# Kernel tuning notes

Hardware: AMD Instinct MI355X
Metric: run time of the kernel (lower is better)

## Reference

```python
import jax, jax.numpy as jnp
import numpy as np

B, NQ, NK, C = 16, 8, 4096, 256
H = W = 64
HEADS = 8
CI = 128          # embedding_dim // attention_downsample_rate
HD = CI // HEADS  # per-head dim
EPS = float(np.finfo(np.float32).tiny)


def _gumbel_topk(scores, noise, n):
    # iterative gumbel-softmax top-k relaxation with straight-through hard k-hot
    g = scores + noise
    khot = jnp.zeros_like(g)
    onehot = jnp.zeros_like(g)
    for _ in range(n):
        g = g + jnp.log(jnp.maximum(1.0 - onehot, EPS))
        onehot = jax.nn.softmax(g, axis=-1)
        khot = khot + onehot
    _, ind = jax.lax.top_k(khot, n)
    rows = jnp.arange(khot.shape[0])[:, None]
    hard = jnp.zeros_like(khot).at[rows, ind].set(1.0)
    ret = hard - jax.lax.stop_gradient(khot) + khot  # == hard numerically
    return ret, jnp.sort(ind, axis=1)  # sorted idx = row-major order of boolean-mask select


def _sample_points(pe, content, ret, idx):
    # pe [H,W,C], content [b,H,W,C], ret [b,HW] k-hot, idx [b,k] sorted
    b = ret.shape[0]
    m = ret.reshape(b, H, W, 1)
    pe_m = (pe[None] * m).reshape(b, H * W, -1)
    c_m = (content * m).reshape(b, H * W, -1)
    take = lambda a: jnp.take_along_axis(a, idx[:, :, None], axis=1)
    return take(pe_m), take(c_m)


def _mlp(x, W1, b1, W2, b2, W3, b3):
    x = jax.nn.relu(x @ W1 + b1)
    x = jax.nn.relu(x @ W2 + b2)
    return x @ W3 + b3


def _forward(queries, keys, query_pe, key_pe, guiding_embedding, gumbel_p, gumbel_n,
             static_uncertain, static_refined, Wq, bq, Wk, bk, Wv, bv, Wo, bo,
             uW1, ub1, uW2, ub2, uW3, ub3, rW1, rb1, rW2, rb2, rW3, rb3,
             pe_gauss, point_pos, point_neg, n_sample_points):
    b = queries.shape[0]
    g = guiding_embedding.reshape(b, C, H * W).transpose(0, 2, 1)  # [b, HW, C]
    g = g * keys  # elementwise gating -> new guiding embedding

    # cross attention token -> image (internal dim CI, HEADS heads)
    def split_heads(x, Wx, bx):
        return (x @ Wx + bx).reshape(b, -1, HEADS, HD).transpose(0, 2, 1, 3)
    qh = split_heads(queries + query_pe, Wq, bq)
    kh = split_heads(g + key_pe, Wk, bk)
    vh = split_heads(g, Wv, bv)
    attn = jax.nn.softmax(jnp.einsum('bhqd,bhkd->bhqk', qh, kh) / np.float32(np.sqrt(HD)), axis=-1)
    out = jnp.einsum('bhqk,bhkd->bhqd', attn, vh).transpose(0, 2, 1, 3).reshape(b, -1, CI)
    queries = out @ Wo + bo  # [b, NQ, C]

    q1 = queries[:, 1, :]
    unc_tok = _mlp(jnp.concatenate([jnp.broadcast_to(static_uncertain, (b, C)), q1], -1),
                   uW1, ub1, uW2, ub2, uW3, ub3)
    ref_tok = _mlp(jnp.concatenate([jnp.broadcast_to(static_refined, (b, C)), q1], -1),
                   rW1, rb1, rW2, rb2, rW3, rb3)

    img = g.transpose(0, 2, 1)  # [b, C, HW]
    unc_norm = jax.nn.sigmoid(jnp.einsum('bc,bcn->bn', unc_tok, img))
    ref_mask = jnp.einsum('bc,bcn->bn', ref_tok, img)
    coarse_mask = jnp.einsum('bc,bcn->bn', q1, img)

    queries = jnp.concatenate([queries[:, 0:1], ref_tok[:, None, :], queries[:, 2:]], axis=1)

    # point-sampling reference map + gumbel-softmax top-k (training-path math)
    ref_map = unc_norm * (jax.nn.sigmoid(ref_mask) - jax.nn.sigmoid(coarse_mask))  # [b, HW]
    ret_p, idx_p = _gumbel_topk(ref_map, gumbel_p, n_sample_points)
    ret_n, idx_n = _gumbel_topk(-ref_map, gumbel_n, n_sample_points)

    # random fourier positional encoding of the 64x64 grid (SAM PositionEmbeddingRandom)
    xs = (jnp.arange(W, dtype=jnp.float32) + 0.5) / W
    ys = (jnp.arange(H, dtype=jnp.float32) + 0.5) / H
    coords = jnp.stack([jnp.tile(xs[None, :], (H, 1)), jnp.tile(ys[:, None], (1, W))], axis=-1)
    proj = ((2.0 * coords - 1.0) @ pe_gauss) * np.float32(2.0 * np.pi)  # [H, W, C//2]
    pe = jnp.concatenate([jnp.sin(proj), jnp.cos(proj)], axis=-1)       # [H, W, C]

    # F.interpolate of a 64x64 map to (64,64) is the identity here
    content = (keys + g).reshape(b, H, W, C)

    sp_pe, sp_c = _sample_points(pe, content, ret_p, idx_p)
    sn_pe, sn_c = _sample_points(pe, content, ret_n, idx_n)
    sp_pe = sp_pe + point_pos  # prompt_encoder.point_embeddings[1]
    sn_pe = sn_pe + point_neg  # prompt_encoder.point_embeddings[0]

    query_pe = jnp.concatenate([query_pe, sp_pe, sn_pe], axis=1)
    queries = jnp.concatenate([queries, sp_c, sn_c], axis=1)
    # pack (queries, query_pe) into one array for a single-output reference
    return jnp.concatenate([queries, query_pe], axis=1)  # [b, 2*(NQ+2k), C]


def setup_inputs():
    key = jax.random.key(0)
    ks = iter(jax.random.split(key, 48))
    n = lambda shape, s=1.0: jax.random.normal(next(ks), shape, jnp.float32) * s
    z = lambda shape: jnp.zeros(shape, jnp.float32)
    return {
        'queries': n((B, NQ, C)),
        'keys': n((B, NK, C)),
        'query_pe': n((B, NQ, C)),
        'key_pe': n((B, NK, C)),
        'guiding_embedding': n((B, C, H, W)),
        'gumbel_p': jax.random.gumbel(next(ks), (B, NK), jnp.float32),
        'gumbel_n': jax.random.gumbel(next(ks), (B, NK), jnp.float32),
        'static_uncertain': n((C,), 0.02),
        'static_refined': n((C,), 0.02),
        'Wq': n((C, CI), 0.02), 'bq': z((CI,)),
        'Wk': n((C, CI), 0.02), 'bk': z((CI,)),
        'Wv': n((C, CI), 0.02), 'bv': z((CI,)),
        'Wo': n((CI, C), 0.02), 'bo': z((C,)),
        'uW1': n((2 * C, C // 4), 0.05), 'ub1': z((C // 4,)),
        'uW2': n((C // 4, C // 4), 0.05), 'ub2': z((C // 4,)),
        'uW3': n((C // 4, C), 0.05), 'ub3': z((C,)),
        'rW1': n((2 * C, C // 4), 0.05), 'rb1': z((C // 4,)),
        'rW2': n((C // 4, C // 4), 0.05), 'rb2': z((C // 4,)),
        'rW3': n((C // 4, C), 0.05), 'rb3': z((C,)),
        'pe_gauss': n((2, C // 2)),
        'point_pos': n((C,), 0.02),
        'point_neg': n((C,), 0.02),
        'n_sample_points': 4,
    }


def reference(queries, keys, query_pe, key_pe, guiding_embedding, gumbel_p, gumbel_n,
              static_uncertain, static_refined, Wq, bq, Wk, bk, Wv, bv, Wo, bo,
              uW1, ub1, uW2, ub2, uW3, ub3, rW1, rb1, rW2, rb2, rW3, rb3,
              pe_gauss, point_pos, point_neg, n_sample_points):
    return _forward(queries, keys, query_pe, key_pe, guiding_embedding, gumbel_p, gumbel_n,
                    static_uncertain, static_refined, Wq, bq, Wk, bk, Wv, bv, Wo, bo,
                    uW1, ub1, uW2, ub2, uW3, ub3, rW1, rb1, rW2, rb2, rW3, rb3,
                    pe_gauss, point_pos, point_neg, n_sample_points)
```

## Files before the change

### kernel.cpp

```cpp
#include <hip/hip_runtime.h>

#define BB 16
#define NQn 8
#define NK 4096
#define CC 256
#define NHEADS 8
#define CIn 128
#define HDn 16
#define NHQ 64
#define EPS_TINY 1.17549435e-38f

constexpr size_t OFF_QK   = 0;
constexpr size_t OFF_QBK  = OFF_QK  + (size_t)BB*CC*NHQ;
constexpr size_t OFF_SC   = OFF_QBK + (size_t)BB*NHQ;
constexpr size_t OFF_MP   = OFF_SC  + (size_t)BB*NK*NHQ;
constexpr size_t OFF_SP   = OFF_MP  + (size_t)BB*16*NHQ;
constexpr size_t OFF_M    = OFF_SP  + (size_t)BB*16*NHQ;
constexpr size_t OFF_RS   = OFF_M   + (size_t)BB*NHQ;
constexpr size_t OFF_AVP  = OFF_RS  + (size_t)BB*NHQ;
constexpr size_t OFF_QATT = OFF_AVP + (size_t)BB*16*NHQ*CC;
constexpr size_t OFF_UNC  = OFF_QATT+ (size_t)BB*NQn*CC;
constexpr size_t OFF_REFT = OFF_UNC + (size_t)BB*CC;
constexpr size_t OFF_RMAP = OFF_REFT+ (size_t)BB*CC;
constexpr size_t OFF_IDX  = OFF_RMAP+ (size_t)BB*NK;
constexpr size_t OFF_RV   = OFF_IDX + 128;
constexpr size_t OFF_G    = OFF_RV  + 128;

__global__ __launch_bounds__(256) void t0_g(
    const float* __restrict__ keys, const float* __restrict__ guiding,
    float* __restrict__ ws)
{
  int bc = blockIdx.y; int b = bc >> 2; int c0 = (bc & 3) * 64;
  int n0 = blockIdx.x * 64; int t = threadIdx.x;
  __shared__ float Gt[64][65];
  int lane = t & 63, grp = t >> 6;
  #pragma unroll
  for (int cc = 0; cc < 16; ++cc) {
    int c = grp*16 + cc;
    Gt[c][lane] = guiding[((size_t)b*CC + c0 + c)*NK + n0 + lane];
  }
  __syncthreads();
  float* G = ws + OFF_G;
  int c4 = (t & 15) * 4, rowg = t >> 4;
  #pragma unroll
  for (int p = 0; p < 4; ++p) {
    int row = p*16 + rowg;
    size_t base = ((size_t)b*NK + n0 + row)*CC + c0 + c4;
    float4 kv = *(const float4*)&keys[base];
    float4 o;
    o.x = kv.x * Gt[c4+0][row];
    o.y = kv.y * Gt[c4+1][row];
    o.z = kv.z * Gt[c4+2][row];
    o.w = kv.w * Gt[c4+3][row];
    *(float4*)&G[base] = o;
  }
}

__global__ __launch_bounds__(256) void k1_qside(
    const float* __restrict__ queries, const float* __restrict__ query_pe,
    const float* __restrict__ Wq, const float* __restrict__ bq,
    const float* __restrict__ Wk, const float* __restrict__ bk,
    float* __restrict__ ws)
{
  int b = blockIdx.x >> 3, q = blockIdx.x & 7, t = threadIdx.x;
  __shared__ float x[CC];
  __shared__ float qh[CIn];
  x[t] = queries[(b*NQn+q)*CC + t] + query_pe[(b*NQn+q)*CC + t];
  __syncthreads();
  if (t < CIn) {
    float a = bq[t];
    for (int c = 0; c < CC; ++c) a += x[c]*Wq[c*CIn + t];
    qh[t] = a * 0.25f;
  }
  __syncthreads();
  float* Qk = ws + OFF_QK;
  #pragma unroll
  for (int h = 0; h < NHEADS; ++h) {
    float a = 0.f;
    #pragma unroll
    for (int d = 0; d < HDn; ++d) a += qh[h*HDn+d] * Wk[t*CIn + h*HDn + d];
    Qk[((size_t)b*CC + t)*NHQ + h*NQn + q] = a;
  }
  if (t < NHEADS) {
    float a = 0.f;
    #pragma unroll
    for (int d = 0; d < HDn; ++d) a += qh[t*HDn+d] * bk[t*HDn+d];
    (ws + OFF_QBK)[b*NHQ + t*NQn + q] = a;
  }
}

__global__ __launch_bounds__(256) void k2_scores(
    const float* __restrict__ key_pe, float* __restrict__ ws)
{
  int b = blockIdx.y, n0 = blockIdx.x * 64, t = threadIdx.x;
  __shared__ __align__(16) float Xs[64][68];
  __shared__ __align__(16) float Qs[64][64];
  const float* Qk = ws + OFF_QK;
  const float* G  = ws + OFF_G;
  int tx = t & 15, ty = t >> 4;
  int c4 = (t & 15)*4, rowg = t >> 4;
  float acc[4][4] = {};
  for (int c0 = 0; c0 < CC; c0 += 64) {
    __syncthreads();
    #pragma unroll
    for (int p = 0; p < 4; ++p) {
      int row = p*16 + rowg;
      size_t base = ((size_t)b*NK + n0 + row)*CC + c0 + c4;
      float4 gv = *(const float4*)&G[base];
      float4 pv = *(const float4*)&key_pe[base];
      float4 o; o.x = gv.x+pv.x; o.y = gv.y+pv.y; o.z = gv.z+pv.z; o.w = gv.w+pv.w;
      *(float4*)&Xs[row][c4] = o;
    }
    #pragma unroll
    for (int i = 0; i < 16; ++i) {
      int l = i*256 + t;
      Qs[l >> 6][l & 63] = Qk[((size_t)b*CC + c0 + (l>>6))*NHQ + (l & 63)];
    }
    __syncthreads();
    #pragma unroll 4
    for (int cb = 0; cb < 16; ++cb) {
      float4 xf[4], qf[4];
      #pragma unroll
      for (int i = 0; i < 4; ++i) xf[i] = *(const float4*)&Xs[4*ty+i][4*cb];
      #pragma unroll
      for (int u = 0; u < 4; ++u) qf[u] = *(const float4*)&Qs[4*cb+u][4*tx];
      #pragma unroll
      for (int u = 0; u < 4; ++u) {
        float xu[4] = { ((const float*)&xf[0])[u], ((const float*)&xf[1])[u],
                        ((const float*)&xf[2])[u], ((const float*)&xf[3])[u] };
        float qu[4] = { qf[u].x, qf[u].y, qf[u].z, qf[u].w };
        #pragma unroll
        for (int i = 0; i < 4; ++i)
          #pragma unroll
          for (int j = 0; j < 4; ++j) acc[i][j] += xu[i]*qu[j];
      }
    }
  }
  const float* qbk = ws + OFF_QBK + (size_t)b*NHQ;
  float qb[4] = {qbk[4*tx], qbk[4*tx+1], qbk[4*tx+2], qbk[4*tx+3]};
  float* sc = ws + OFF_SC + ((size_t)b*NK + n0)*NHQ;
  #pragma unroll
  for (int i = 0; i < 4; ++i) {
    float4 o;
    o.x = acc[i][0]+qb[0]; o.y = acc[i][1]+qb[1]; o.z = acc[i][2]+qb[2]; o.w = acc[i][3]+qb[3];
    *(float4*)&sc[(4*ty + i)*NHQ + 4*tx] = o;
  }
}

__global__ __launch_bounds__(256) void k3a_stats(float* __restrict__ ws)
{
  int b = blockIdx.y, sb = blockIdx.x, t = threadIdx.x;
  int hq = t & 63, r = t >> 6;
  const float* sc = ws + OFF_SC + ((size_t)b*NK + sb*256)*NHQ;
  float m = -INFINITY, s = 0.f;
  for (int i = 0; i < 64; ++i) {
    float v = sc[(r + 4*i)*NHQ + hq];
    if (v > m) { s = s*expf(m - v) + 1.f; m = v; } else { s += expf(v - m); }
  }
  __shared__ float rm[256], rs[256];
  rm[t] = m; rs[t] = s;
  __syncthreads();
  if (t < 64) {
    float m0=rm[t], m1=rm[t+64], m2=rm[t+128], m3=rm[t+192];
    float mm = fmaxf(fmaxf(m0,m1), fmaxf(m2,m3));
    float ss = rs[t]*expf(m0-mm) + rs[t+64]*expf(m1-mm) + rs[t+128]*expf(m2-mm) + rs[t+192]*expf(m3-mm);
    (ws + OFF_MP)[(b*16 + sb)*NHQ + t] = mm;
    (ws + OFF_SP)[(b*16 + sb)*NHQ + t] = ss;
  }
}

__global__ __launch_bounds__(64) void k3b_combine(float* __restrict__ ws)
{
  int b = blockIdx.x, hq = threadIdx.x;
  const float* mp = ws + OFF_MP + (size_t)b*16*NHQ;
  const float* sp = ws + OFF_SP + (size_t)b*16*NHQ;
  float m = -INFINITY;
  #pragma unroll
  for (int i = 0; i < 16; ++i) m = fmaxf(m, mp[i*NHQ+hq]);
  float s = 0.f;
  #pragma unroll
  for (int i = 0; i < 16; ++i) s += sp[i*NHQ+hq]*expf(mp[i*NHQ+hq]-m);
  (ws+OFF_M)[b*NHQ+hq] = m;
  (ws+OFF_RS)[b*NHQ+hq] = 1.0f/s;
}

__global__ __launch_bounds__(256) void k4_av(float* __restrict__ ws)
{
  int b = blockIdx.y, kb = blockIdx.x, t = threadIdx.x;
  int k0 = kb * 256;
  __shared__ __align__(16) float gld[32][260];
  __shared__ __align__(16) float wld[32][64];
  __shared__ float mv[64], rv[64];
  if (t < 64) { mv[t] = (ws+OFF_M)[b*NHQ+t]; rv[t] = (ws+OFF_RS)[b*NHQ+t]; }
  int th = t & 15, tc = t >> 4;
  float accf[4][16] = {};
  const float* sc = ws + OFF_SC;
  const float* G  = ws + OFF_G;
  for (int kk = 0; kk < 256; kk += 32) {
    __syncthreads();
    #pragma unroll
    for (int p = 0; p < 8; ++p) {
      int row = (t>>6) + 4*p;
      *(float4*)&gld[row][(t&63)*4] =
        *(const float4*)&G[((size_t)b*NK + k0+kk+row)*CC + (t&63)*4];
    }
    #pragma unroll
    for (int i = 0; i < 8; ++i) {
      int l = i*256 + t; int k = l >> 6, hq = l & 63;
      float v = sc[((size_t)b*NK + k0+kk+k)*NHQ + hq];
      wld[k][hq] = expf(v - mv[hq]) * rv[hq];
    }
    __syncthreads();
    for (int k = 0; k < 32; ++k) {
      float4 w4 = *(const float4*)&wld[k][4*th];
      float4 g0 = *(const float4*)&gld[k][16*tc];
      float4 g1 = *(const float4*)&gld[k][16*tc+4];
      float4 g2 = *(const float4*)&gld[k][16*tc+8];
      float4 g3 = *(const float4*)&gld[k][16*tc+12];
      float wq[4] = {w4.x, w4.y, w4.z, w4.w};
      float gq[16] = {g0.x,g0.y,g0.z,g0.w, g1.x,g1.y,g1.z,g1.w,
                      g2.x,g2.y,g2.z,g2.w, g3.x,g3.y,g3.z,g3.w};
      #pragma unroll
      for (int i = 0; i < 4; ++i)
        #pragma unroll
        for (int j = 0; j < 16; ++j) accf[i][j] += wq[i]*gq[j];
    }
  }
  float* avp = ws + OFF_AVP + (((size_t)b*16 + kb)*NHQ)*CC;
  #pragma unroll
  for (int i = 0; i < 4; ++i)
    #pragma unroll
    for (int j4 = 0; j4 < 4; ++j4) {
      float4 o;
      o.x = accf[i][4*j4]; o.y = accf[i][4*j4+1]; o.z = accf[i][4*j4+2]; o.w = accf[i][4*j4+3];
      *(float4*)&avp[(4*th + i)*CC + 16*tc + 4*j4] = o;
    }
}

__global__ __launch_bounds__(256) void k56_attout(
    const float* __restrict__ Wv, const float* __restrict__ bv,
    const float* __restrict__ Wo, const float* __restrict__ bo,
    float* __restrict__ ws)
{
  int b = blockIdx.x >> 3, q = blockIdx.x & 7, t = threadIdx.x;
  __shared__ float avs[NHEADS][CC];
  __shared__ float outv[CIn];
  const float* avp = ws + OFF_AVP;
  #pragma unroll
  for (int h = 0; h < NHEADS; ++h) {
    int hq = h*NQn + q;
    float a = 0.f;
    #pragma unroll 4
    for (int kb = 0; kb < 16; ++kb)
      a += avp[(((size_t)b*16 + kb)*NHQ + hq)*CC + t];
    avs[h][t] = a;
  }
  __syncthreads();
  if (t < CIn) {
    int h = t >> 4;
    float a = bv[t];
    for (int c = 0; c < CC; ++c) a += avs[h][c]*Wv[c*CIn + t];
    outv[t] = a;
  }
  __syncthreads();
  float a = bo[t];
  for (int ci = 0; ci < CIn; ++ci) a += outv[ci]*Wo[ci*CC + t];
  (ws+OFF_QATT)[((size_t)b*NQn + q)*CC + t] = a;
}

__global__ __launch_bounds__(256) void k7_mlps(
    const float* __restrict__ su, const float* __restrict__ sr,
    const float* __restrict__ uW1, const float* __restrict__ ub1,
    const float* __restrict__ uW2, const float* __restrict__ ub2,
    const float* __restrict__ uW3, const float* __restrict__ ub3,
    const float* __restrict__ rW1, const float* __restrict__ rb1,
    const float* __restrict__ rW2, const float* __restrict__ rb2,
    const float* __restrict__ rW3, const float* __restrict__ rb3,
    float* __restrict__ ws)
{
  int b = blockIdx.x, t = threadIdx.x;
  __shared__ float xs[768];
  __shared__ float h1[2][64], h2[2][64];
  xs[t] = su[t];
  xs[256+t] = (ws+OFF_QATT)[((size_t)b*NQn + 1)*CC + t];
  xs[512+t] = sr[t];
  __syncthreads();
  if (t < 128) {
    int which = t >> 6, o = t & 63;
    const float* W1 = which ? rW1 : uW1;
    const float* b1 = which ? rb1 : ub1;
    int base = which ? 512 : 0;
    float a = b1[o];
    for (int i = 0; i < 256; ++i) a += xs[base+i]*W1[i*64 + o];
    for (int i = 0; i < 256; ++i) a += xs[256+i]*W1[(256+i)*64 + o];
    h1[which][o] = fmaxf(a, 0.f);
  }
  __syncthreads();
  if (t < 128) {
    int which = t >> 6, o = t & 63;
    const float* W2 = which ? rW2 : uW2;
    const float* b2 = which ? rb2 : ub2;
    float a = b2[o];
    #pragma unroll 8
    for (int i = 0; i < 64; ++i) a += h1[which][i]*W2[i*64+o];
    h2[which][o] = fmaxf(a, 0.f);
  }
  __syncthreads();
  {
    float a = ub3[t];
    #pragma unroll 8
    for (int i = 0; i < 64; ++i) a += h2[0][i]*uW3[i*CC + t];
    (ws+OFF_UNC)[b*CC + t] = a;
    float a2 = rb3[t];
    #pragma unroll 8
    for (int i = 0; i < 64; ++i) a2 += h2[1][i]*rW3[i*CC + t];
    (ws+OFF_REFT)[b*CC + t] = a2;
  }
}

__global__ __launch_bounds__(256) void k8_masks(float* __restrict__ ws)
{
  int b = blockIdx.y, t = threadIdx.x;
  int wave = t >> 6, lane = t & 63;
  __shared__ float q1s[CC], us[CC], rts[CC];
  q1s[t] = (ws+OFF_QATT)[((size_t)b*NQn+1)*CC + t];
  us[t]  = (ws+OFF_UNC)[b*CC + t];
  rts[t] = (ws+OFF_REFT)[b*CC + t];
  __syncthreads();
  float q1v[4], usv[4], rtv[4];
  #pragma unroll
  for (int u = 0; u < 4; ++u) {
    q1v[u] = q1s[lane*4+u]; usv[u] = us[lane*4+u]; rtv[u] = rts[lane*4+u];
  }
  const float* G = ws + OFF_G;
  float* rmap = ws + OFF_RMAP + (size_t)b*NK;
  int n_base = blockIdx.x*64 + wave*16;
  for (int r = 0; r < 16; ++r) {
    int n = n_base + r;
    float4 gv = *(const float4*)&G[((size_t)b*NK + n)*CC + lane*4];
    float aq = gv.x*q1v[0] + gv.y*q1v[1] + gv.z*q1v[2] + gv.w*q1v[3];
    float au = gv.x*usv[0] + gv.y*usv[1] + gv.z*usv[2] + gv.w*usv[3];
    float ar = gv.x*rtv[0] + gv.y*rtv[1] + gv.z*rtv[2] + gv.w*rtv[3];
    #pragma unroll
    for (int s = 1; s < 64; s <<= 1) {
      aq += __shfl_xor(aq, s, 64);
      au += __shfl_xor(au, s, 64);
      ar += __shfl_xor(ar, s, 64);
    }
    if (lane == 0) {
      float un = 1.f/(1.f+expf(-au));
      rmap[n] = un * (1.f/(1.f+expf(-ar)) - 1.f/(1.f+expf(-aq)));
    }
  }
}

__global__ __launch_bounds__(256) void k9_gumbel(
    const float* __restrict__ gp, const float* __restrict__ gn,
    float* __restrict__ ws)
{
  int sign = blockIdx.x, b = blockIdx.y, t = threadIdx.x;
  const float* noise = sign ? gn : gp;
  const float* rmap = ws + OFF_RMAP + (size_t)b*NK;
  float g[16], kh[16], oh[16];
  #pragma unroll
  for (int i = 0; i < 16; ++i) {
    int n = i*256 + t;
    float scv = rmap[n];
    if (sign) scv = -scv;
    g[i] = scv + noise[(size_t)b*NK + n];
    kh[i] = 0.f; oh[i] = 0.f;
  }
  __shared__ float rv[256];
  __shared__ int ri[256];
  for (int it = 0; it < 4; ++it) {
    if (it > 0) {
      #pragma unroll
      for (int i = 0; i < 16; ++i) g[i] += logf(fmaxf(1.f - oh[i], EPS_TINY));
    }
    float m = g[0];
    #pragma unroll
    for (int i = 1; i < 16; ++i) m = fmaxf(m, g[i]);
    rv[t] = m; __syncthreads();
    for (int s = 128; s > 0; s >>= 1) { if (t < s) rv[t] = fmaxf(rv[t], rv[t+s]); __syncthreads(); }
    m = rv[0]; __syncthreads();
    float e[16], ls = 0.f;
    #pragma unroll
    for (int i = 0; i < 16; ++i) { e[i] = expf(g[i]-m); ls += e[i]; }
    rv[t] = ls; __syncthreads();
    for (int s = 128; s > 0; s >>= 1) { if (t < s) rv[t] += rv[t+s]; __syncthreads(); }
    float ssum = rv[0]; __syncthreads();
    #pragma unroll
    for (int i = 0; i < 16; ++i) { oh[i] = e[i]/ssum; kh[i] += oh[i]; }
  }
  __shared__ int selI[4]; __shared__ float selR[4];
  for (int j = 0; j < 4; ++j) {
    float bvv = kh[0]; int bii = t;
    #pragma unroll
    for (int i = 1; i < 16; ++i) {
      if (kh[i] > bvv) { bvv = kh[i]; bii = i*256 + t; }
    }
    rv[t] = bvv; ri[t] = bii; __syncthreads();
    for (int s = 128; s > 0; s >>= 1) {
      if (t < s) {
        float v2 = rv[t+s]; int i2 = ri[t+s];
        if (v2 > rv[t] || (v2 == rv[t] && i2 < ri[t])) { rv[t] = v2; ri[t] = i2; }
      }
      __syncthreads();
    }
    int bidx = ri[0]; float bkh = rv[0];
    if (t == 0) { selI[j] = bidx; selR[j] = (1.f - bkh) + bkh; }
    if (t == (bidx & 255)) {
      int slot = bidx >> 8;
      #pragma unroll
      for (int i = 0; i < 16; ++i) if (i == slot) kh[i] = -1.f;
    }
    __syncthreads();
  }
  if (t == 0) {
    int id[4]; float rr[4];
    #pragma unroll
    for (int j = 0; j < 4; ++j) { id[j] = selI[j]; rr[j] = selR[j]; }
    for (int a = 0; a < 3; ++a)
      for (int c2 = a+1; c2 < 4; ++c2)
        if (id[c2] < id[a]) { int ti=id[a]; id[a]=id[c2]; id[c2]=ti; float tr=rr[a]; rr[a]=rr[c2]; rr[c2]=tr; }
    int* iout = (int*)(ws + OFF_IDX);
    float* rout = ws + OFF_RV;
    for (int j = 0; j < 4; ++j) {
      iout[(sign*BB + b)*4 + j] = id[j];
      rout[(sign*BB + b)*4 + j] = rr[j];
    }
  }
}

__global__ __launch_bounds__(256) void k10_out(
    const float* __restrict__ keys, const float* __restrict__ query_pe,
    const float* __restrict__ point_pos, const float* __restrict__ point_neg,
    const float* __restrict__ pe_gauss,
    float* __restrict__ ws, float* __restrict__ out)
{
  int b = blockIdx.y, r = blockIdx.x, t = threadIdx.x;
  const float* G = ws + OFF_G;
  float val;
  if (r < 8) {
    val = (r == 1) ? (ws+OFF_REFT)[b*CC + t]
                   : (ws+OFF_QATT)[((size_t)b*NQn + r)*CC + t];
  } else if (r < 16) {
    int j = r - 8; int sign = j >> 2; int jj = j & 3;
    int idx = ((const int*)(ws+OFF_IDX))[(sign*BB + b)*4 + jj];
    float rvv = (ws+OFF_RV)[(sign*BB + b)*4 + jj];
    float kv = keys[((size_t)b*NK + idx)*CC + t];
    float gv = G[((size_t)b*NK + idx)*CC + t];
    val = (kv + gv) * rvv;
  } else if (r < 24) {
    val = query_pe[((size_t)b*NQn + (r-16))*CC + t];
  } else {
    int j = r - 24; int sign = j >> 2; int jj = j & 3;
    int idx = ((const int*)(ws+OFF_IDX))[(sign*BB + b)*4 + jj];
    float rvv = (ws+OFF_RV)[(sign*BB + b)*4 + jj];
    const float* point = sign ? point_neg : point_pos;
    int h = idx >> 6, w = idx & 63;
    float x = (w + 0.5f)/64.f, y = (h + 0.5f)/64.f;
    int jf = (t < 128) ? t : (t - 128);
    float proj = ((2.f*x - 1.f)*pe_gauss[jf] + (2.f*y - 1.f)*pe_gauss[128 + jf]) * 6.28318530717958647692f;
    float sv = (t < 128) ? sinf(proj) : cosf(proj);
    val = sv*rvv + point[t];
  }
  out[((size_t)b*32 + r)*CC + t] = val;
}

extern "C" void kernel_launch(void* const* d_in, const int* in_sizes, int n_in,
                              void* d_out, int out_size, void* d_ws, size_t ws_size,
                              hipStream_t stream)
{
  const float* queries   = (const float*)d_in[0];
  const float* keys      = (const float*)d_in[1];
  const float* query_pe  = (const float*)d_in[2];
  const float* key_pe    = (const float*)d_in[3];
  const float* guiding   = (const float*)d_in[4];
  const float* gumbel_p  = (const float*)d_in[5];
  const float* gumbel_n  = (const float*)d_in[6];
  const float* s_unc     = (const float*)d_in[7];
  const float* s_ref     = (const float*)d_in[8];
  const float* Wq  = (const float*)d_in[9];   const float* bq  = (const float*)d_in[10];
  const float* Wk  = (const float*)d_in[11];  const float* bk  = (const float*)d_in[12];
  const float* Wv  = (const float*)d_in[13];  const float* bv  = (const float*)d_in[14];
  const float* Wo  = (const float*)d_in[15];  const float* bo  = (const float*)d_in[16];
  const float* uW1 = (const float*)d_in[17];  const float* ub1 = (const float*)d_in[18];
  const float* uW2 = (const float*)d_in[19];  const float* ub2 = (const float*)d_in[20];
  const float* uW3 = (const float*)d_in[21];  const float* ub3 = (const float*)d_in[22];
  const float* rW1 = (const float*)d_in[23];  const float* rb1 = (const float*)d_in[24];
  const float* rW2 = (const float*)d_in[25];  const float* rb2 = (const float*)d_in[26];
  const float* rW3 = (const float*)d_in[27];  const float* rb3 = (const float*)d_in[28];
  const float* pe_gauss  = (const float*)d_in[29];
  const float* point_pos = (const float*)d_in[30];
  const float* point_neg = (const float*)d_in[31];
  float* ws = (float*)d_ws;
  float* out = (float*)d_out;

  t0_g      <<<dim3(64, 64),  256, 0, stream>>>(keys, guiding, ws);
  k1_qside  <<<dim3(BB*NQn),  256, 0, stream>>>(queries, query_pe, Wq, bq, Wk, bk, ws);
  k2_scores <<<dim3(64, BB),  256, 0, stream>>>(key_pe, ws);
  k3a_stats <<<dim3(16, BB),  256, 0, stream>>>(ws);
  k3b_combine<<<dim3(BB),      64, 0, stream>>>(ws);
  k4_av     <<<dim3(16, BB),  256, 0, stream>>>(ws);
  k56_attout<<<dim3(BB*NQn),  256, 0, stream>>>(Wv, bv, Wo, bo, ws);
  k7_mlps   <<<dim3(BB),      256, 0, stream>>>(s_unc, s_ref, uW1, ub1, uW2, ub2, uW3, ub3,
                                                rW1, rb1, rW2, rb2, rW3, rb3, ws);
  k8_masks  <<<dim3(64, BB),  256, 0, stream>>>(ws);
  k9_gumbel <<<dim3(2, BB),   256, 0, stream>>>(gumbel_p, gumbel_n, ws);
  k10_out   <<<dim3(32, BB),  256, 0, stream>>>(keys, query_pe, point_pos, point_neg,
                                                pe_gauss, ws, out);
}
```

Before: 254.7 us.

## Fuse guiding gating into score kernel and widen AV kernel to 512 threads

Removes the separate t0_g kernel. The score kernel now computes the gated embedding G = keys*guiding on the fly through a shared-memory transpose, writes G out for later kernels, and uses it directly for the key projection. This avoids one round trip of reading G back from global memory and saves a launch. Separately, k4_av moves to 512 threads per block with a smaller 8x4 per-thread accumulator tile, trading register pressure and arithmetic intensity per thread for more waves per block.

```diff
diff --git a/kernel.cpp b/kernel.cpp
--- a/kernel.cpp
+++ b/kernel.cpp
@@ -26,36 +26,6 @@
 constexpr size_t OFF_RV   = OFF_IDX + 128;
 constexpr size_t OFF_G    = OFF_RV  + 128;
 
-__global__ __launch_bounds__(256) void t0_g(
-    const float* __restrict__ keys, const float* __restrict__ guiding,
-    float* __restrict__ ws)
-{
-  int bc = blockIdx.y; int b = bc >> 2; int c0 = (bc & 3) * 64;
-  int n0 = blockIdx.x * 64; int t = threadIdx.x;
-  __shared__ float Gt[64][65];
-  int lane = t & 63, grp = t >> 6;
-  #pragma unroll
-  for (int cc = 0; cc < 16; ++cc) {
-    int c = grp*16 + cc;
-    Gt[c][lane] = guiding[((size_t)b*CC + c0 + c)*NK + n0 + lane];
-  }
-  __syncthreads();
-  float* G = ws + OFF_G;
-  int c4 = (t & 15) * 4, rowg = t >> 4;
-  #pragma unroll
-  for (int p = 0; p < 4; ++p) {
-    int row = p*16 + rowg;
-    size_t base = ((size_t)b*NK + n0 + row)*CC + c0 + c4;
-    float4 kv = *(const float4*)&keys[base];
-    float4 o;
-    o.x = kv.x * Gt[c4+0][row];
-    o.y = kv.y * Gt[c4+1][row];
-    o.z = kv.z * Gt[c4+2][row];
-    o.w = kv.w * Gt[c4+3][row];
-    *(float4*)&G[base] = o;
-  }
-}
-
 __global__ __launch_bounds__(256) void k1_qside(
     const float* __restrict__ queries, const float* __restrict__ query_pe,
     const float* __restrict__ Wq, const float* __restrict__ bq,
@@ -90,31 +60,46 @@
 }
 
 __global__ __launch_bounds__(256) void k2_scores(
-    const float* __restrict__ key_pe, float* __restrict__ ws)
+    const float* __restrict__ keys, const float* __restrict__ key_pe,
+    const float* __restrict__ guiding, float* __restrict__ ws)
 {
   int b = blockIdx.y, n0 = blockIdx.x * 64, t = threadIdx.x;
   __shared__ __align__(16) float Xs[64][68];
   __shared__ __align__(16) float Qs[64][64];
+  __shared__ float Gt[64][65];
   const float* Qk = ws + OFF_QK;
-  const float* G  = ws + OFF_G;
+  float* G = ws + OFF_G;
   int tx = t & 15, ty = t >> 4;
   int c4 = (t & 15)*4, rowg = t >> 4;
+  int lane = t & 63, grp = t >> 6;
   float acc[4][4] = {};
   for (int c0 = 0; c0 < CC; c0 += 64) {
+    __syncthreads();
+    #pragma unroll
+    for (int cc = 0; cc < 16; ++cc) {
+      int c = grp*16 + cc;
+      Gt[c][lane] = guiding[((size_t)b*CC + c0 + c)*NK + n0 + lane];
+    }
+    #pragma unroll
+    for (int i = 0; i < 16; ++i) {
+      int l = i*256 + t;
+      Qs[l >> 6][l & 63] = Qk[((size_t)b*CC + c0 + (l>>6))*NHQ + (l & 63)];
+    }
     __syncthreads();
     #pragma unroll
     for (int p = 0; p < 4; ++p) {
       int row = p*16 + rowg;
       size_t base = ((size_t)b*NK + n0 + row)*CC + c0 + c4;
-      float4 gv = *(const float4*)&G[base];
+      float4 kv = *(const float4*)&keys[base];
       float4 pv = *(const float4*)&key_pe[base];
-      float4 o; o.x = gv.x+pv.x; o.y = gv.y+pv.y; o.z = gv.z+pv.z; o.w = gv.w+pv.w;
+      float4 g4;
+      g4.x = kv.x * Gt[c4+0][row];
+      g4.y = kv.y * Gt[c4+1][row];
+      g4.z = kv.z * Gt[c4+2][row];
+      g4.w = kv.w * Gt[c4+3][row];
+      *(float4*)&G[base] = g4;
+      float4 o; o.x = g4.x+pv.x; o.y = g4.y+pv.y; o.z = g4.z+pv.z; o.w = g4.w+pv.w;
       *(float4*)&Xs[row][c4] = o;
-    }
-    #pragma unroll
-    for (int i = 0; i < 16; ++i) {
-      int l = i*256 + t;
-      Qs[l >> 6][l & 63] = Qk[((size_t)b*CC + c0 + (l>>6))*NHQ + (l & 63)];
     }
     __syncthreads();
     #pragma unroll 4
@@ -184,7 +169,7 @@
   (ws+OFF_RS)[b*NHQ+hq] = 1.0f/s;
 }
 
-__global__ __launch_bounds__(256) void k4_av(float* __restrict__ ws)
+__global__ __launch_bounds__(512) void k4_av(float* __restrict__ ws)
 {
   int b = blockIdx.y, kb = blockIdx.x, t = threadIdx.x;
   int k0 = kb * 256;
@@ -192,49 +177,45 @@
   __shared__ __align__(16) float wld[32][64];
   __shared__ float mv[64], rv[64];
   if (t < 64) { mv[t] = (ws+OFF_M)[b*NHQ+t]; rv[t] = (ws+OFF_RS)[b*NHQ+t]; }
-  int th = t & 15, tc = t >> 4;
-  float accf[4][16] = {};
+  int hq0 = (t & 7) * 8, c0 = (t >> 3) * 4;
+  float accf[8][4] = {};
   const float* sc = ws + OFF_SC;
   const float* G  = ws + OFF_G;
   for (int kk = 0; kk < 256; kk += 32) {
     __syncthreads();
     #pragma unroll
-    for (int p = 0; p < 8; ++p) {
-      int row = (t>>6) + 4*p;
+    for (int p = 0; p < 4; ++p) {
+      int row = p*8 + (t>>6);
       *(float4*)&gld[row][(t&63)*4] =
         *(const float4*)&G[((size_t)b*NK + k0+kk+row)*CC + (t&63)*4];
     }
     #pragma unroll
-    for (int i = 0; i < 8; ++i) {
-      int l = i*256 + t; int k = l >> 6, hq = l & 63;
+    for (int i = 0; i < 4; ++i) {
+      int l = i*512 + t; int k = l >> 6, hq = l & 63;
       float v = sc[((size_t)b*NK + k0+kk+k)*NHQ + hq];
       wld[k][hq] = expf(v - mv[hq]) * rv[hq];
     }
     __syncthreads();
+    #pragma unroll 2
     for (int k = 0; k < 32; ++k) {
-      float4 w4 = *(const float4*)&wld[k][4*th];
-      float4 g0 = *(const float4*)&gld[k][16*tc];
-      float4 g1 = *(const float4*)&gld[k][16*tc+4];
-      float4 g2 = *(const float4*)&gld[k][16*tc+8];
-      float4 g3 = *(const float4*)&gld[k][16*tc+12];
-      float wq[4] = {w4.x, w4.y, w4.z, w4.w};
-      float gq[16] = {g0.x,g0.y,g0.z,g0.w, g1.x,g1.y,g1.z,g1.w,
-                      g2.x,g2.y,g2.z,g2.w, g3.x,g3.y,g3.z,g3.w};
-      #pragma unroll
-      for (int i = 0; i < 4; ++i)
+      float4 w0 = *(const float4*)&wld[k][hq0];
+      float4 w1 = *(const float4*)&wld[k][hq0+4];
+      float4 gv = *(const float4*)&gld[k][c0];
+      float wq[8] = {w0.x,w0.y,w0.z,w0.w, w1.x,w1.y,w1.z,w1.w};
+      float gq[4] = {gv.x,gv.y,gv.z,gv.w};
+      #pragma unroll
+      for (int i = 0; i < 8; ++i)
         #pragma unroll
-        for (int j = 0; j < 16; ++j) accf[i][j] += wq[i]*gq[j];
+        for (int j = 0; j < 4; ++j) accf[i][j] += wq[i]*gq[j];
     }
   }
   float* avp = ws + OFF_AVP + (((size_t)b*16 + kb)*NHQ)*CC;
   #pragma unroll
-  for (int i = 0; i < 4; ++i)
-    #pragma unroll
-    for (int j4 = 0; j4 < 4; ++j4) {
-      float4 o;
-      o.x = accf[i][4*j4]; o.y = accf[i][4*j4+1]; o.z = accf[i][4*j4+2]; o.w = accf[i][4*j4+3];
-      *(float4*)&avp[(4*th + i)*CC + 16*tc + 4*j4] = o;
-    }
+  for (int i = 0; i < 8; ++i) {
+    float4 o;
+    o.x = accf[i][0]; o.y = accf[i][1]; o.z = accf[i][2]; o.w = accf[i][3];
+    *(float4*)&avp[(size_t)(hq0 + i)*CC + c0] = o;
+  }
 }
 
 __global__ __launch_bounds__(256) void k56_attout(
@@ -497,12 +478,11 @@
   float* ws = (float*)d_ws;
   float* out = (float*)d_out;
 
-  t0_g      <<<dim3(64, 64),  256, 0, stream>>>(keys, guiding, ws);
   k1_qside  <<<dim3(BB*NQn),  256, 0, stream>>>(queries, query_pe, Wq, bq, Wk, bk, ws);
-  k2_scores <<<dim3(64, BB),  256, 0, stream>>>(key_pe, ws);
+  k2_scores <<<dim3(64, BB),  256, 0, stream>>>(keys, key_pe, guiding, ws);
   k3a_stats <<<dim3(16, BB),  256, 0, stream>>>(ws);
   k3b_combine<<<dim3(BB),      64, 0, stream>>>(ws);
-  k4_av     <<<dim3(16, BB),  256, 0, stream>>>(ws);
+  k4_av     <<<dim3(16, BB),  512, 0, stream>>>(ws);
   k56_attout<<<dim3(BB*NQn),  256, 0, stream>>>(Wv, bv, Wo, bo, ws);
   k7_mlps   <<<dim3(BB),      256, 0, stream>>>(s_unc, s_ref, uW1, ub1, uW2, ub2, uW3, ub3,
                                                 rW1, rb1, rW2, rb2, rW3, rb3, ws);
```

New measurement: 249.5 us. 2.1% less time.
